# Kernel tuning notes

Measured on AMD Instinct MI355X. Metric: run time of the kernel, lower is better.

## Reference

```python
import jax, jax.numpy as jnp
import numpy as np


def setup_inputs() -> dict:
    key = jax.random.key(0)
    ks = jax.random.split(key, 9)
    N, L, E, H = 8, 4096, 1024, 16
    D = E // H
    return {
        "values": jax.random.normal(ks[0], (N, L, E), dtype=jnp.float32),
        "keys": jax.random.normal(ks[1], (N, L, E), dtype=jnp.float32),
        "query": jax.random.normal(ks[2], (N, L, E), dtype=jnp.float32),
        "mask": jax.random.randint(ks[3], (1, 1, H, H), 0, 2, dtype=jnp.int32),
        "Wv": jax.random.normal(ks[4], (D, D), dtype=jnp.float32) / np.sqrt(D),
        "Wk": jax.random.normal(ks[5], (D, D), dtype=jnp.float32) / np.sqrt(D),
        "Wq": jax.random.normal(ks[6], (D, D), dtype=jnp.float32) / np.sqrt(D),
        "Wo": jax.random.normal(ks[7], (E, E), dtype=jnp.float32) / np.sqrt(E),
        "bo": jnp.zeros((E,), dtype=jnp.float32),
    }


def reference(values, keys, query, mask, Wv, Wk, Wq, Wo, bo):
    N, L, E = query.shape
    H = mask.shape[-1]          # heads
    D = E // H                  # head_dim
    # reshape to (N, L, H, D) then per-head Dense(head_dim) on last dim
    v = values.reshape(N, L, H, D) @ Wv
    k = keys.reshape(N, L, H, D) @ Wk
    q = query.reshape(N, L, H, D) @ Wq
    # Faithful to the source: keys transposed with perm [0,1,3,2], so matmul
    # batches over (N, L) and energy is a (H x H) matrix per position.
    energy = jnp.einsum("nlhd,nlgd->nlhg", q, k)  # (N, L, H, H)
    energy = jnp.where(mask == 0, jnp.float32(-1e20), energy)
    attention = jax.nn.softmax(energy / (E ** 0.5), axis=-1)
    out = jnp.einsum("nlhg,nlgd->nlhd", attention, v)  # (N, L, H, D)
    # source: transpose to (N, H, L, D) then reshape to (N, L, H*D)
    out = out.transpose(0, 2, 1, 3).reshape(N, L, H * D)
    out = out @ Wo + bo
    return out, attention
```

## Files before the change

### kernel.cpp

```cpp
#include <hip/hip_runtime.h>

typedef short short8 __attribute__((ext_vector_type(8)));
typedef float f32x4 __attribute__((ext_vector_type(4)));
typedef unsigned short u16;

#define MFMA16(a, b, c) __builtin_amdgcn_mfma_f32_16x16x32_bf16(a, b, c, 0, 0, 0)
#define GLD_LDS(g, l)                                                          \
  __builtin_amdgcn_global_load_lds(                                            \
      (__attribute__((address_space(1))) void*)(void*)(g),                     \
      (__attribute__((address_space(3))) void*)(l), 16, 0, 0)

__device__ __forceinline__ u16 f2bf(float f) {
  union { float f; unsigned u; } x; x.f = f;
  unsigned r = x.u + 0x7fffu + ((x.u >> 16) & 1u);
  return (u16)(r >> 16);
}

__device__ __forceinline__ short8 pack8(float4 a, float4 b) {
  short8 r;
  r[0] = (short)f2bf(a.x); r[1] = (short)f2bf(a.y);
  r[2] = (short)f2bf(a.z); r[3] = (short)f2bf(a.w);
  r[4] = (short)f2bf(b.x); r[5] = (short)f2bf(b.y);
  r[6] = (short)f2bf(b.z); r[7] = (short)f2bf(b.w);
  return r;
}

__global__ __launch_bounds__(256) void prep(const float* __restrict__ Wv,
                                            const float* __restrict__ Wk,
                                            const float* __restrict__ Wq,
                                            const float* __restrict__ Wo,
                                            u16* __restrict__ WoT2,
                                            u16* __restrict__ Mt) {
  __shared__ __align__(16) float A[64][65];
  __shared__ __align__(16) float B[64][68];
  const int t = threadIdx.x;
  const int r = t >> 2, c = (t & 3) * 16;
  if (blockIdx.x < 256) {
    const int tr = blockIdx.x >> 4, tc = blockIdx.x & 15;
#pragma unroll
    for (int u = 0; u < 4; ++u)
      *(float4*)&A[r][c + u * 4] = *(const float4*)(Wv + r * 64 + c + u * 4);
#pragma unroll
    for (int u = 0; u < 4; ++u)
      *(float4*)&B[r][c + u * 4] =
          *(const float4*)(Wo + (tr * 64 + r) * 1024 + tc * 64 + c + u * 4);
    __syncthreads();
    const int n = t & 63, i0 = (t >> 6) * 16;
    float acc[16];
#pragma unroll
    for (int ii = 0; ii < 16; ++ii) acc[ii] = 0.f;
    for (int j = 0; j < 64; ++j) {
      const float wo = B[j][n];
#pragma unroll
      for (int ii = 0; ii < 16; ++ii) acc[ii] += A[i0 + ii][j] * wo;
    }
    u16* dst = WoT2 + (size_t)(tc * 64 + n) * 1024 + tr * 64 + i0;
    short8 o0, o1;
#pragma unroll
    for (int jj = 0; jj < 8; ++jj) { o0[jj] = (short)f2bf(acc[jj]); o1[jj] = (short)f2bf(acc[8 + jj]); }
    *(short8*)(void*)dst = o0;
    *(short8*)(void*)(dst + 8) = o1;
  } else {
#pragma unroll
    for (int u = 0; u < 4; ++u)
      *(float4*)&A[r][c + u * 4] = *(const float4*)(Wq + r * 64 + c + u * 4);
#pragma unroll
    for (int u = 0; u < 4; ++u)
      *(float4*)&B[r][c + u * 4] = *(const float4*)(Wk + r * 64 + c + u * 4);
    __syncthreads();
    const int n = t & 63, k0 = (t >> 6) * 16;
    float acc[16];
#pragma unroll
    for (int ii = 0; ii < 16; ++ii) acc[ii] = 0.f;
    for (int d = 0; d < 64; ++d) {
      const float wk = B[n][d];
#pragma unroll
      for (int kk = 0; kk < 16; ++kk) acc[kk] += A[k0 + kk][d] * wk;
    }
    u16* dst = Mt + n * 64 + k0;
    short8 o0, o1;
#pragma unroll
    for (int jj = 0; jj < 8; ++jj) { o0[jj] = (short)f2bf(acc[jj]); o1[jj] = (short)f2bf(acc[8 + jj]); }
    *(short8*)(void*)dst = o0;
    *(short8*)(void*)(dst + 8) = o1;
  }
}

__global__ __launch_bounds__(256, 4) void attn_kernel(
    const float* __restrict__ values, const float* __restrict__ keys,
    const float* __restrict__ query, const int* __restrict__ mask,
    const u16* __restrict__ Mt, float* __restrict__ attn,
    u16* __restrict__ out2) {
  __shared__ __align__(16) u16 t_lds[4][16][72];
  __shared__ __align__(16) u16 vT_lds[4][64][24];
  __shared__ __align__(16) u16 p_lds[4][16][24];

  const int tid = threadIdx.x;
  const int w = tid >> 6, lane = tid & 63;
  const int g16 = lane & 15;
  const int q4 = lane >> 4;
  const int kbase = q4 * 8;
  const int mrow = q4 * 4;

  short8 mtf[2][4];
#pragma unroll
  for (int kb = 0; kb < 2; ++kb)
#pragma unroll
    for (int nc = 0; nc < 4; ++nc)
      mtf[kb][nc] =
          *(const short8*)(Mt + (nc * 16 + g16) * 64 + kb * 32 + kbase);

  bool mz[4];
#pragma unroll
  for (int r = 0; r < 4; ++r) mz[r] = (mask[(mrow + r) * 16 + g16] == 0);

  const f32x4 zero = {0.f, 0.f, 0.f, 0.f};
  const int gw = blockIdx.x * 4 + w;

#define LD4(dst, src, off)                                                     \
  {                                                                            \
    dst[0] = *(const float4*)((src) + (off));                                  \
    dst[1] = *(const float4*)((src) + (off) + 4);                              \
    dst[2] = *(const float4*)((src) + (off) + 32);                             \
    dst[3] = *(const float4*)((src) + (off) + 36);                             \
  }

  float4 qr[4], kr[4], vr[4];
  {
    const int off0 = gw * 8 * 1024 + g16 * 64 + kbase;
    LD4(qr, query, off0);
    LD4(kr, keys, off0);
  }

#pragma unroll 1
  for (int i = 0; i < 8; ++i) {
    const int p = gw * 8 + i;
    const int off = p * 1024 + g16 * 64 + kbase;
    LD4(vr, values, off);

    short8 aq0 = pack8(qr[0], qr[1]), aq1 = pack8(qr[2], qr[3]);
    short8 ak0 = pack8(kr[0], kr[1]), ak1 = pack8(kr[2], kr[3]);

    if (i < 7) {
      LD4(qr, query, off + 1024);
      LD4(kr, keys, off + 1024);
    }

    f32x4 tacc[4];
#pragma unroll
    for (int nc = 0; nc < 4; ++nc) {
      tacc[nc] = MFMA16(aq0, mtf[0][nc], zero);
      tacc[nc] = MFMA16(aq1, mtf[1][nc], tacc[nc]);
    }
#pragma unroll
    for (int nc = 0; nc < 4; ++nc)
#pragma unroll
      for (int r = 0; r < 4; ++r)
        t_lds[w][mrow + r][nc * 16 + g16] = f2bf(tacc[nc][r]);

    short8 ea0 = *(const short8*)&t_lds[w][g16][kbase];
    short8 ea1 = *(const short8*)&t_lds[w][g16][32 + kbase];
    f32x4 acce = MFMA16(ea0, ak0, zero);
    acce = MFMA16(ea1, ak1, acce);

    float av4[4];
#pragma unroll
    for (int r = 0; r < 4; ++r) {
      const float val = mz[r] ? -30.f : acce[r] * 0.03125f;
      const float pe = __expf(val);
      float s = pe;
      s += __shfl_xor(s, 1, 16);
      s += __shfl_xor(s, 2, 16);
      s += __shfl_xor(s, 4, 16);
      s += __shfl_xor(s, 8, 16);
      av4[r] = pe * __builtin_amdgcn_rcpf(s);
    }

    short8 av0 = pack8(vr[0], vr[1]), av1 = pack8(vr[2], vr[3]);
#pragma unroll
    for (int j = 0; j < 8; ++j) {
      vT_lds[w][kbase + j][g16] = av0[j];
      vT_lds[w][32 + kbase + j][g16] = av1[j];
    }

    float* ap = attn + (size_t)p * 256 + mrow * 16 + g16;
#pragma unroll
    for (int r = 0; r < 4; ++r) {
      ap[r * 16] = av4[r];
      p_lds[w][mrow + r][g16] = f2bf(av4[r]);
    }

    short8 pa;
    if (lane < 32) {
      pa = *(const short8*)&p_lds[w][g16][kbase];
    } else {
      short8 z = {0, 0, 0, 0, 0, 0, 0, 0};
      pa = z;
    }
    const int gsel = (lane < 32) ? kbase : 0;
    const int nn = p >> 12, l = p & 4095;
    u16* op = out2 + ((nn * 4096 + (l >> 4)) * 1024) + (l & 15) * 64;
#pragma unroll
    for (int nc = 0; nc < 4; ++nc) {
      short8 vb = *(const short8*)&vT_lds[w][nc * 16 + g16][gsel];
      f32x4 acco = MFMA16(pa, vb, zero);
#pragma unroll
      for (int r = 0; r < 4; ++r)
        op[(mrow + r) * 262144 + nc * 16 + g16] = f2bf(acco[r]);
    }
  }
#undef LD4
}

__global__ __launch_bounds__(256, 2) void gemm_kernel(
    const u16* __restrict__ A, const u16* __restrict__ BT,
    const float* __restrict__ bo, float* __restrict__ C) {
  __shared__ __align__(16) u16 As[128 * 32];
  __shared__ __align__(16) u16 Bs[128 * 32];
  const int t = threadIdx.x, lane = t & 63;
  const int g16 = lane & 15, q4 = lane >> 4;
  const int w = t >> 6, wm = w >> 1, wn = w & 1;
  const int bm = blockIdx.x & 255, bn = blockIdx.x >> 8;

  f32x4 acc[4][4];
  const f32x4 zero = {0.f, 0.f, 0.f, 0.f};
#pragma unroll
  for (int mt = 0; mt < 4; ++mt)
#pragma unroll
    for (int nt = 0; nt < 4; ++nt) acc[mt][nt] = zero;

  const int am = t >> 2, ak = (t & 3) * 8;
  const u16* ga = A + (size_t)(bm * 128 + am) * 1024 + ak;
  const u16* gb = BT + (size_t)(bn * 128 + am) * 1024 + ak;
  u16* lA = &As[t * 8];
  u16* lB = &Bs[t * 8];

  for (int kt = 0; kt < 32; ++kt) {
    __syncthreads();
    const int ko = kt * 32;
    GLD_LDS(ga + ko, lA);
    GLD_LDS(ga + 64 * 1024 + ko, lA + 2048);
    GLD_LDS(gb + ko, lB);
    GLD_LDS(gb + 64 * 1024 + ko, lB + 2048);
    __syncthreads();

    short8 af[4], bf[4];
#pragma unroll
    for (int mt = 0; mt < 4; ++mt)
      af[mt] = *(const short8*)&As[(wm * 64 + mt * 16 + g16) * 32 + q4 * 8];
#pragma unroll
    for (int nt = 0; nt < 4; ++nt)
      bf[nt] = *(const short8*)&Bs[(wn * 64 + nt * 16 + g16) * 32 + q4 * 8];
#pragma unroll
    for (int mt = 0; mt < 4; ++mt)
#pragma unroll
      for (int nt = 0; nt < 4; ++nt)
        acc[mt][nt] = MFMA16(af[mt], bf[nt], acc[mt][nt]);
  }

#pragma unroll
  for (int nt = 0; nt < 4; ++nt) {
    const int col = bn * 128 + wn * 64 + nt * 16 + g16;
    const float bias = bo[col];
#pragma unroll
    for (int mt = 0; mt < 4; ++mt) {
#pragma unroll
      for (int r = 0; r < 4; ++r) {
        const int row = bm * 128 + wm * 64 + mt * 16 + q4 * 4 + r;
        C[(size_t)row * 1024 + col] = acc[mt][nt][r] + bias;
      }
    }
  }
}

extern "C" void kernel_launch(void* const* d_in, const int* in_sizes, int n_in,
                              void* d_out, int out_size, void* d_ws,
                              size_t ws_size, hipStream_t stream) {
  const float* values = (const float*)d_in[0];
  const float* keys   = (const float*)d_in[1];
  const float* query  = (const float*)d_in[2];
  const int*   mask   = (const int*)d_in[3];
  const float* Wv = (const float*)d_in[4];
  const float* Wk = (const float*)d_in[5];
  const float* Wq = (const float*)d_in[6];
  const float* Wo = (const float*)d_in[7];
  const float* bo = (const float*)d_in[8];

  float* out  = (float*)d_out;
  float* attn = out + 33554432;

  u16* out2 = (u16*)d_ws;
  u16* WoT2 = out2 + 33554432;
  u16* Mt   = WoT2 + 1048576;

  prep<<<257, 256, 0, stream>>>(Wv, Wk, Wq, Wo, WoT2, Mt);
  attn_kernel<<<1024, 256, 0, stream>>>(values, keys, query, mask, Mt, attn,
                                        out2);
  gemm_kernel<<<2048, 256, 0, stream>>>(out2, WoT2, bo, out);
}
```

Before: 262.6 us.

## Coalesce attention output stores and fold head transpose into GEMM A addressing

```diff
diff --git a/kernel.cpp b/kernel.cpp
--- a/kernel.cpp
+++ b/kernel.cpp
@@ -86,7 +86,7 @@
   }
 }
 
-__global__ __launch_bounds__(256, 4) void attn_kernel(
+__global__ __launch_bounds__(256, 3) void attn_kernel(
     const float* __restrict__ values, const float* __restrict__ keys,
     const float* __restrict__ query, const int* __restrict__ mask,
     const u16* __restrict__ Mt, float* __restrict__ attn,
@@ -125,25 +125,24 @@
     dst[3] = *(const float4*)((src) + (off) + 36);                             \
   }
 
-  float4 qr[4], kr[4], vr[4];
-  {
-    const int off0 = gw * 8 * 1024 + g16 * 64 + kbase;
-    LD4(qr, query, off0);
-    LD4(kr, keys, off0);
-  }
+  float4 qs[4], ks[4], vs[4];
+  const int off0 = gw * 8 * 1024 + g16 * 64 + kbase;
+  LD4(qs, query, off0);
+  LD4(ks, keys, off0);
+  LD4(vs, values, off0);
 
 #pragma unroll 1
   for (int i = 0; i < 8; ++i) {
     const int p = gw * 8 + i;
-    const int off = p * 1024 + g16 * 64 + kbase;
-    LD4(vr, values, off);
-
-    short8 aq0 = pack8(qr[0], qr[1]), aq1 = pack8(qr[2], qr[3]);
-    short8 ak0 = pack8(kr[0], kr[1]), ak1 = pack8(kr[2], kr[3]);
-
+
+    short8 aq0 = pack8(qs[0], qs[1]), aq1 = pack8(qs[2], qs[3]);
+    short8 ak0 = pack8(ks[0], ks[1]), ak1 = pack8(ks[2], ks[3]);
+    short8 av0 = pack8(vs[0], vs[1]), av1 = pack8(vs[2], vs[3]);
     if (i < 7) {
-      LD4(qr, query, off + 1024);
-      LD4(kr, keys, off + 1024);
+      const int off = off0 + (i + 1) * 1024;
+      LD4(qs, query, off);
+      LD4(ks, keys, off);
+      LD4(vs, values, off);
     }
 
     f32x4 tacc[4];
@@ -157,17 +156,24 @@
 #pragma unroll
       for (int r = 0; r < 4; ++r)
         t_lds[w][mrow + r][nc * 16 + g16] = f2bf(tacc[nc][r]);
+
+#pragma unroll
+    for (int j = 0; j < 8; ++j) {
+      vT_lds[w][kbase + j][g16] = av0[j];
+      vT_lds[w][32 + kbase + j][g16] = av1[j];
+    }
 
     short8 ea0 = *(const short8*)&t_lds[w][g16][kbase];
     short8 ea1 = *(const short8*)&t_lds[w][g16][32 + kbase];
     f32x4 acce = MFMA16(ea0, ak0, zero);
     acce = MFMA16(ea1, ak1, acce);
 
+    const float SC = 0.045084220027780106f;
     float av4[4];
 #pragma unroll
     for (int r = 0; r < 4; ++r) {
-      const float val = mz[r] ? -30.f : acce[r] * 0.03125f;
-      const float pe = __expf(val);
+      const float val = mz[r] ? -45.f : acce[r] * SC;
+      const float pe = exp2f(val);
       float s = pe;
       s += __shfl_xor(s, 1, 16);
       s += __shfl_xor(s, 2, 16);
@@ -176,13 +182,6 @@
       av4[r] = pe * __builtin_amdgcn_rcpf(s);
     }
 
-    short8 av0 = pack8(vr[0], vr[1]), av1 = pack8(vr[2], vr[3]);
-#pragma unroll
-    for (int j = 0; j < 8; ++j) {
-      vT_lds[w][kbase + j][g16] = av0[j];
-      vT_lds[w][32 + kbase + j][g16] = av1[j];
-    }
-
     float* ap = attn + (size_t)p * 256 + mrow * 16 + g16;
 #pragma unroll
     for (int r = 0; r < 4; ++r) {
@@ -198,16 +197,21 @@
       pa = z;
     }
     const int gsel = (lane < 32) ? kbase : 0;
-    const int nn = p >> 12, l = p & 4095;
-    u16* op = out2 + ((nn * 4096 + (l >> 4)) * 1024) + (l & 15) * 64;
 #pragma unroll
     for (int nc = 0; nc < 4; ++nc) {
       short8 vb = *(const short8*)&vT_lds[w][nc * 16 + g16][gsel];
       f32x4 acco = MFMA16(pa, vb, zero);
 #pragma unroll
       for (int r = 0; r < 4; ++r)
-        op[(mrow + r) * 262144 + nc * 16 + g16] = f2bf(acco[r]);
-    }
+        t_lds[w][mrow + r][nc * 16 + g16] = f2bf(acco[r]);
+    }
+
+    const u16* orow = &t_lds[w][lane >> 2][(lane & 3) * 16];
+    short8 s0 = *(const short8*)orow;
+    short8 s1 = *(const short8*)(orow + 8);
+    u16* dst = out2 + (size_t)p * 1024 + lane * 16;
+    *(short8*)(void*)dst = s0;
+    *(short8*)(void*)(dst + 8) = s1;
   }
 #undef LD4
 }
@@ -230,16 +234,26 @@
     for (int nt = 0; nt < 4; ++nt) acc[mt][nt] = zero;
 
   const int am = t >> 2, ak = (t & 3) * 8;
-  const u16* ga = A + (size_t)(bm * 128 + am) * 1024 + ak;
+  const int R0 = bm * 128 + am;
+  const int R1 = R0 + 64;
+  const size_t base0 =
+      ((size_t)((R0 >> 12) * 4096 + (R0 & 255) * 16)) * 1024 +
+      ((R0 & 4095) >> 8) * 64;
+  const size_t base1 =
+      ((size_t)((R1 >> 12) * 4096 + (R1 & 255) * 16)) * 1024 +
+      ((R1 & 4095) >> 8) * 64;
+  const u16* ga0 = A + base0 + ak;
+  const u16* ga1 = A + base1 + ak;
   const u16* gb = BT + (size_t)(bn * 128 + am) * 1024 + ak;
   u16* lA = &As[t * 8];
   u16* lB = &Bs[t * 8];
 
   for (int kt = 0; kt < 32; ++kt) {
     __syncthreads();
+    const int aoff = (kt >> 1) * 1024 + (kt & 1) * 32;
     const int ko = kt * 32;
-    GLD_LDS(ga + ko, lA);
-    GLD_LDS(ga + 64 * 1024 + ko, lA + 2048);
+    GLD_LDS(ga0 + aoff, lA);
+    GLD_LDS(ga1 + aoff, lA + 2048);
     GLD_LDS(gb + ko, lB);
     GLD_LDS(gb + 64 * 1024 + ko, lB + 2048);
     __syncthreads();
```

After: 238.1 us. -9.3%, faster.
